# Optimization experiments

Hardware: AMD Instinct MI355X
Metric: run time of the kernel (lower is better)

Reference implementation:

```python
import jax, jax.numpy as jnp
import numpy as np

S, D = 8192, 2048      # sequence length, feature dim (input_size)
H, E, K, L = 64, 64, 2, 64  # gate hidden, expert count, top-k, expert layer_size
EPS = 1e-12            # torch F.normalize eps


def setup_inputs() -> dict:
    key = jax.random.key(0)
    ks = jax.random.split(key, 5)
    x = jax.random.normal(ks[0], (S, D), dtype=jnp.float32)
    # torch nn.Linear weights have shape [out_features, in_features]
    Wg_in = jax.random.normal(ks[1], (H, D), dtype=jnp.float32) * 0.02   # gate.input
    Wg_lin = jax.random.normal(ks[2], (E, H), dtype=jnp.float32) * 0.02  # gate.linear
    Wg_out = jax.random.normal(ks[3], (1, S), dtype=jnp.float32) * 0.02  # gate.output
    We = jax.random.normal(ks[4], (E, L, D), dtype=jnp.float32) * 0.02   # expert weight bank
    return {"x": x, "Wg_in": Wg_in, "Wg_lin": Wg_lin, "Wg_out": Wg_out, "We": We}


def reference(x, Wg_in, Wg_lin, Wg_out, We):
    # --- SparseGate (eval mode: dropout = identity) ---
    h = x @ Wg_in.T                         # [S, H]
    logits = h @ Wg_lin.T                   # [S, E]
    scores = (logits.T @ Wg_out.T)[:, 0]    # Linear(S,1) applied to [E,S] -> [E]
    topv, idx = jax.lax.top_k(scores, K)    # global top-k experts for whole input
    g = jax.nn.softmax(topv)                # softmax over the k selected logits

    # --- dispatch to k selected experts (FFNN: Linear -> normalize(-1) -> GELU) ---
    Wsel = We[idx]                          # [K, L, D]
    z = jnp.einsum('sd,kld->ksl', x, Wsel)  # [K, S, L]
    z = z / jnp.maximum(jnp.linalg.norm(z, axis=-1, keepdims=True), EPS)
    z = jax.nn.gelu(z, approximate=False)   # torch GELU default is exact erf

    # --- weighted combine: sum_k g_k * expert_k(x) ---
    return jnp.einsum('k,ksl->sl', g, z)    # [S, L]
```

## Files before the change

kernel.cpp:

```cpp
#include <hip/hip_runtime.h>
#include <hip/hip_bf16.h>
#include <math.h>

#define D_DIM 2048
#define L_DIM 64
#define E_NUM 64
#define H_DIM 64

typedef float f32x4_t __attribute__((ext_vector_type(4)));
typedef __bf16 bf16x8_t __attribute__((ext_vector_type(8)));

#define WS_UPART 0u
#define WS_U     (128u * 2048u * 4u)
#define WS_V     (WS_U + 2048u * 4u)
#define WS_META  (WS_V + 256u)
#define WS_WB    (WS_META + 64u)

__global__ void k_upart(const float* __restrict__ x, const float* __restrict__ wout,
                        float* __restrict__ upart) {
  const int d4 = (blockIdx.x * 256 + threadIdx.x) * 4;
  const int s0 = blockIdx.y * 64;
  const float* xp = x + (size_t)s0 * D_DIM + d4;
  float4 acc = make_float4(0.f, 0.f, 0.f, 0.f);
#pragma unroll 8
  for (int i = 0; i < 64; ++i) {
    const float w = wout[s0 + i];
    const float4 xv = *reinterpret_cast<const float4*>(xp + (size_t)i * D_DIM);
    acc.x += xv.x * w; acc.y += xv.y * w; acc.z += xv.z * w; acc.w += xv.w * w;
  }
  *reinterpret_cast<float4*>(upart + (size_t)blockIdx.y * D_DIM + d4) = acc;
}

__global__ void k_ufinish(const float* __restrict__ upart, float* __restrict__ u) {
  const int d = blockIdx.x * 256 + threadIdx.x;
  float s = 0.f;
#pragma unroll 8
  for (int c = 0; c < 128; ++c) s += upart[(size_t)c * D_DIM + d];
  u[d] = s;
}

__global__ void k_v(const float* __restrict__ wg_in, const float* __restrict__ u,
                    float* __restrict__ v) {
  const int h = blockIdx.x;
  const int t = threadIdx.x;
  const float4* wr = reinterpret_cast<const float4*>(wg_in + (size_t)h * D_DIM);
  const float4* ur = reinterpret_cast<const float4*>(u);
  float s = 0.f;
#pragma unroll
  for (int i = t; i < 512; i += 256) {
    const float4 a = wr[i];
    const float4 b = ur[i];
    s += a.x * b.x + a.y * b.y + a.z * b.z + a.w * b.w;
  }
  __shared__ float red[4];
#pragma unroll
  for (int off = 32; off; off >>= 1) s += __shfl_down(s, off, 64);
  if ((t & 63) == 0) red[t >> 6] = s;
  __syncthreads();
  if (t == 0) v[h] = red[0] + red[1] + red[2] + red[3];
}

__global__ void k_gate(const float* __restrict__ wg_lin, const float* __restrict__ v,
                       int* __restrict__ sel, float* __restrict__ g) {
  __shared__ float vv[H_DIM];
  __shared__ float sc[E_NUM];
  const int t = threadIdx.x;
  vv[t] = v[t];
  __syncthreads();
  float s = 0.f;
#pragma unroll 8
  for (int hh = 0; hh < H_DIM; ++hh) s += wg_lin[t * H_DIM + hh] * vv[hh];
  sc[t] = s;
  __syncthreads();
  if (t == 0) {
    int b1 = 0; float m1 = sc[0];
    for (int e = 1; e < E_NUM; ++e) { if (sc[e] > m1) { m1 = sc[e]; b1 = e; } }
    int b2 = -1; float m2 = -3.4e38f;
    for (int e = 0; e < E_NUM; ++e) {
      if (e != b1 && sc[e] > m2) { m2 = sc[e]; b2 = e; }
    }
    const float e2 = expf(m2 - m1);
    const float g0 = 1.0f / (1.0f + e2);
    sel[0] = b1; sel[1] = b2;
    g[0] = g0; g[1] = 1.0f - g0;
  }
}

__global__ void k_wb(const float* __restrict__ we, const int* __restrict__ sel,
                     __hip_bfloat16* __restrict__ wb) {
  const int n = blockIdx.x;
  const int e = sel[n >> 6];
  const int l = n & 63;
  const float* src = we + ((size_t)e * L_DIM + l) * D_DIM;
  const int t = threadIdx.x;
  const float4 a = reinterpret_cast<const float4*>(src)[2 * t];
  const float4 b = reinterpret_cast<const float4*>(src)[2 * t + 1];
  union { __hip_bfloat16 h[8]; uint4 u; } pk;
  pk.h[0] = __float2bfloat16(a.x); pk.h[1] = __float2bfloat16(a.y);
  pk.h[2] = __float2bfloat16(a.z); pk.h[3] = __float2bfloat16(a.w);
  pk.h[4] = __float2bfloat16(b.x); pk.h[5] = __float2bfloat16(b.y);
  pk.h[6] = __float2bfloat16(b.z); pk.h[7] = __float2bfloat16(b.w);
  reinterpret_cast<uint4*>(wb + (size_t)n * D_DIM)[t] = pk.u;
}

__device__ __forceinline__ void async_ld16(const void* gp, void* lp) {
  __builtin_amdgcn_global_load_lds(
      (const __attribute__((address_space(1))) unsigned int*)gp,
      (__attribute__((address_space(3))) unsigned int*)lp, 16, 0, 0);
}

__device__ __forceinline__ float gelu_f(float v) {
  return 0.5f * v * (1.0f + erff(v * 0.70710678118654752440f));
}

#define STG_BYTES 20992

__global__ __launch_bounds__(1024) void k_moe_gemm(
    const float* __restrict__ x, const __hip_bfloat16* __restrict__ wb,
    const float* __restrict__ gw, float* __restrict__ out) {
  __shared__ __align__(16) unsigned char lds[4 * STG_BYTES];

  const int tid = threadIdx.x;
  const int kg = tid >> 8;
  const int lt = tid & 255;
  const int wc = (tid >> 6) & 3;
  const int lane = tid & 63;
  const int m0 = blockIdx.x * 32;
  const float g0 = gw[0], g1 = gw[1];

  unsigned char* ldsA0 = lds + kg * STG_BYTES;
  unsigned char* ldsB0 = ldsA0 + 32 * 144;

  const int ar = lt >> 3, ac = lt & 7;
  const float* gA = x + (size_t)(m0 + ar) * D_DIM + kg * 512 + ac * 8;
  unsigned char* ldsAw = ldsA0 + ar * 144 + ac * 16;

  const int fr = lane & 15, fq = lane >> 4;

  f32x4_t acc00 = {0.f, 0.f, 0.f, 0.f};
  f32x4_t acc01 = acc00, acc10 = acc00, acc11 = acc00;

  for (int kk = 0; kk < 8; ++kk) {
    const int k0 = kg * 512 + kk * 64;
    if (kk) __syncthreads();
    const float4 a0 = *reinterpret_cast<const float4*>(gA + kk * 64);
    const float4 a1 = *reinterpret_cast<const float4*>(gA + kk * 64 + 4);
    union { __hip_bfloat16 h[8]; uint4 u; } pk;
    pk.h[0] = __float2bfloat16(a0.x); pk.h[1] = __float2bfloat16(a0.y);
    pk.h[2] = __float2bfloat16(a0.z); pk.h[3] = __float2bfloat16(a0.w);
    pk.h[4] = __float2bfloat16(a1.x); pk.h[5] = __float2bfloat16(a1.y);
    pk.h[6] = __float2bfloat16(a1.z); pk.h[7] = __float2bfloat16(a1.w);
    *reinterpret_cast<uint4*>(ldsAw) = pk.u;
#pragma unroll
    for (int i = 0; i < 4; ++i) {
      const int c = i * 256 + lt;
      const int r = c >> 3, p = c & 7;
      const int kc = p ^ (r & 7);
      async_ld16(wb + (size_t)r * D_DIM + k0 + kc * 8, ldsB0 + c * 16);
    }
    __syncthreads();
    union fragu { uint4 u; bf16x8_t v; };
    fragu af[2][2], bfr[2][2];
#pragma unroll
    for (int mt = 0; mt < 2; ++mt)
#pragma unroll
      for (int ks = 0; ks < 2; ++ks)
        af[mt][ks].u = *reinterpret_cast<const uint4*>(
            ldsA0 + (mt * 16 + fr) * 144 + ks * 64 + fq * 16);
#pragma unroll
    for (int nt = 0; nt < 2; ++nt)
#pragma unroll
      for (int ks = 0; ks < 2; ++ks) {
        const int r = wc * 32 + nt * 16 + fr;
        const int kq = ks * 4 + fq;
        bfr[nt][ks].u = *reinterpret_cast<const uint4*>(
            ldsB0 + r * 128 + ((kq ^ (r & 7)) * 16));
      }
    acc00 = __builtin_amdgcn_mfma_f32_16x16x32_bf16(af[0][0].v, bfr[0][0].v, acc00, 0, 0, 0);
    acc00 = __builtin_amdgcn_mfma_f32_16x16x32_bf16(af[0][1].v, bfr[0][1].v, acc00, 0, 0, 0);
    acc01 = __builtin_amdgcn_mfma_f32_16x16x32_bf16(af[0][0].v, bfr[1][0].v, acc01, 0, 0, 0);
    acc01 = __builtin_amdgcn_mfma_f32_16x16x32_bf16(af[0][1].v, bfr[1][1].v, acc01, 0, 0, 0);
    acc10 = __builtin_amdgcn_mfma_f32_16x16x32_bf16(af[1][0].v, bfr[0][0].v, acc10, 0, 0, 0);
    acc10 = __builtin_amdgcn_mfma_f32_16x16x32_bf16(af[1][1].v, bfr[0][1].v, acc10, 0, 0, 0);
    acc11 = __builtin_amdgcn_mfma_f32_16x16x32_bf16(af[1][0].v, bfr[1][0].v, acc11, 0, 0, 0);
    acc11 = __builtin_amdgcn_mfma_f32_16x16x32_bf16(af[1][1].v, bfr[1][1].v, acc11, 0, 0, 0);
  }
  __syncthreads();
  {
    float* z = reinterpret_cast<float*>(lds) + kg * (32 * 132);
    const int colbase = wc * 32 + fr;
#pragma unroll
    for (int reg = 0; reg < 4; ++reg) {
      const int r0 = fq * 4 + reg;
      z[r0 * 132 + colbase]             = acc00[reg];
      z[r0 * 132 + colbase + 16]        = acc01[reg];
      z[(16 + r0) * 132 + colbase]      = acc10[reg];
      z[(16 + r0) * 132 + colbase + 16] = acc11[reg];
    }
  }
  __syncthreads();
  {
    float* zb = reinterpret_cast<float*>(lds);
    const int r = tid >> 5;
    const int cb = (tid & 31) * 4;
    const int o = r * 132 + cb;
    f32x4_t s = *reinterpret_cast<f32x4_t*>(zb + o)
              + *reinterpret_cast<f32x4_t*>(zb + 1 * 4224 + o)
              + *reinterpret_cast<f32x4_t*>(zb + 2 * 4224 + o)
              + *reinterpret_cast<f32x4_t*>(zb + 3 * 4224 + o);
    *reinterpret_cast<f32x4_t*>(zb + o) = s;
  }
  __syncthreads();
  float* z = reinterpret_cast<float*>(lds);
  float* ps = reinterpret_cast<float*>(lds + 4 * 16896);
  if (tid < 256) {
    const int r = tid >> 3, seg = tid & 7;
    float s = 0.f;
#pragma unroll
    for (int i2 = 0; i2 < 16; ++i2) {
      const float t2 = z[r * 132 + seg * 16 + i2];
      s += t2 * t2;
    }
    ps[r * 8 + seg] = s;
  }
  __syncthreads();
  if (tid < 256) {
    const int r = tid >> 3, j = tid & 7;
    const float s0 = ps[r * 8 + 0] + ps[r * 8 + 1] + ps[r * 8 + 2] + ps[r * 8 + 3];
    const float s1 = ps[r * 8 + 4] + ps[r * 8 + 5] + ps[r * 8 + 6] + ps[r * 8 + 7];
    const float i0 = 1.0f / fmaxf(sqrtf(s0), 1e-12f);
    const float i1 = 1.0f / fmaxf(sqrtf(s1), 1e-12f);
    float o[8];
#pragma unroll
    for (int i2 = 0; i2 < 8; ++i2) {
      const int c = j * 8 + i2;
      const float za = z[r * 132 + c] * i0;
      const float zb = z[r * 132 + 64 + c] * i1;
      o[i2] = g0 * gelu_f(za) + g1 * gelu_f(zb);
    }
    float4* op = reinterpret_cast<float4*>(out + (size_t)(m0 + r) * 64 + j * 8);
    op[0] = make_float4(o[0], o[1], o[2], o[3]);
    op[1] = make_float4(o[4], o[5], o[6], o[7]);
  }
}

extern "C" void kernel_launch(void* const* d_in, const int* in_sizes, int n_in,
                              void* d_out, int out_size, void* d_ws, size_t ws_size,
                              hipStream_t stream) {
  (void)in_sizes; (void)n_in; (void)out_size; (void)ws_size;
  const float* x      = (const float*)d_in[0];
  const float* wg_in  = (const float*)d_in[1];
  const float* wg_lin = (const float*)d_in[2];
  const float* wg_out = (const float*)d_in[3];
  const float* we     = (const float*)d_in[4];
  float* out = (float*)d_out;
  char* ws = (char*)d_ws;

  float* upart = (float*)(ws + WS_UPART);
  float* u     = (float*)(ws + WS_U);
  float* v     = (float*)(ws + WS_V);
  int*   sel   = (int*)(ws + WS_META);
  float* g     = (float*)(ws + WS_META + 8);
  __hip_bfloat16* wb = (__hip_bfloat16*)(ws + WS_WB);

  k_upart  <<<dim3(2, 128), 256, 0, stream>>>(x, wg_out, upart);
  k_ufinish<<<8, 256, 0, stream>>>(upart, u);
  k_v      <<<64, 256, 0, stream>>>(wg_in, u, v);
  k_gate   <<<1, 64, 0, stream>>>(wg_lin, v, sel, g);
  k_wb     <<<128, 256, 0, stream>>>(we, sel, wb);
  k_moe_gemm<<<256, 1024, 0, stream>>>(x, wb, g, out);
}
```

Before: 159.3 us.

## Precompute bf16 copy of x in reduction pass and feed it to expert GEMM

```diff
diff --git a/kernel.cpp b/kernel.cpp
--- a/kernel.cpp
+++ b/kernel.cpp
@@ -8,6 +8,7 @@
 #define H_DIM 64
 
 typedef float f32x4_t __attribute__((ext_vector_type(4)));
+typedef unsigned int u32x4_t __attribute__((ext_vector_type(4)));
 typedef __bf16 bf16x8_t __attribute__((ext_vector_type(8)));
 
 #define WS_UPART 0u
@@ -15,18 +16,24 @@
 #define WS_V     (WS_U + 2048u * 4u)
 #define WS_META  (WS_V + 256u)
 #define WS_WB    (WS_META + 64u)
+#define WS_XB    (WS_WB + 128u * 2048u * 2u)
 
 __global__ void k_upart(const float* __restrict__ x, const float* __restrict__ wout,
-                        float* __restrict__ upart) {
+                        float* __restrict__ upart, __hip_bfloat16* __restrict__ xb) {
   const int d4 = (blockIdx.x * 256 + threadIdx.x) * 4;
   const int s0 = blockIdx.y * 64;
   const float* xp = x + (size_t)s0 * D_DIM + d4;
   float4 acc = make_float4(0.f, 0.f, 0.f, 0.f);
-#pragma unroll 8
+#pragma unroll 4
   for (int i = 0; i < 64; ++i) {
     const float w = wout[s0 + i];
-    const float4 xv = *reinterpret_cast<const float4*>(xp + (size_t)i * D_DIM);
-    acc.x += xv.x * w; acc.y += xv.y * w; acc.z += xv.z * w; acc.w += xv.w * w;
+    const f32x4_t xv = __builtin_nontemporal_load(
+        reinterpret_cast<const f32x4_t*>(xp + (size_t)i * D_DIM));
+    acc.x += xv[0] * w; acc.y += xv[1] * w; acc.z += xv[2] * w; acc.w += xv[3] * w;
+    union { __hip_bfloat16 h[4]; uint2 u; } pk;
+    pk.h[0] = __float2bfloat16(xv[0]); pk.h[1] = __float2bfloat16(xv[1]);
+    pk.h[2] = __float2bfloat16(xv[2]); pk.h[3] = __float2bfloat16(xv[3]);
+    *reinterpret_cast<uint2*>(xb + (size_t)(s0 + i) * D_DIM + d4) = pk.u;
   }
   *reinterpret_cast<float4*>(upart + (size_t)blockIdx.y * D_DIM + d4) = acc;
 }
@@ -113,10 +120,10 @@
   return 0.5f * v * (1.0f + erff(v * 0.70710678118654752440f));
 }
 
-#define STG_BYTES 20992
+#define STG_BYTES 20480
 
 __global__ __launch_bounds__(1024) void k_moe_gemm(
-    const float* __restrict__ x, const __hip_bfloat16* __restrict__ wb,
+    const __hip_bfloat16* __restrict__ xb, const __hip_bfloat16* __restrict__ wb,
     const float* __restrict__ gw, float* __restrict__ out) {
   __shared__ __align__(16) unsigned char lds[4 * STG_BYTES];
 
@@ -129,11 +136,12 @@
   const float g0 = gw[0], g1 = gw[1];
 
   unsigned char* ldsA0 = lds + kg * STG_BYTES;
-  unsigned char* ldsB0 = ldsA0 + 32 * 144;
-
-  const int ar = lt >> 3, ac = lt & 7;
-  const float* gA = x + (size_t)(m0 + ar) * D_DIM + kg * 512 + ac * 8;
-  unsigned char* ldsAw = ldsA0 + ar * 144 + ac * 16;
+  unsigned char* ldsB0 = ldsA0 + 32 * 128;
+
+  const int sar = lt >> 3, sap = lt & 7;
+  const int sakc = sap ^ (sar & 7);
+  const __hip_bfloat16* gA = xb + (size_t)(m0 + sar) * D_DIM + kg * 512 + sakc * 8;
+  unsigned char* ldsAw = ldsA0 + lt * 16;
 
   const int fr = lane & 15, fq = lane >> 4;
 
@@ -143,14 +151,8 @@
   for (int kk = 0; kk < 8; ++kk) {
     const int k0 = kg * 512 + kk * 64;
     if (kk) __syncthreads();
-    const float4 a0 = *reinterpret_cast<const float4*>(gA + kk * 64);
-    const float4 a1 = *reinterpret_cast<const float4*>(gA + kk * 64 + 4);
-    union { __hip_bfloat16 h[8]; uint4 u; } pk;
-    pk.h[0] = __float2bfloat16(a0.x); pk.h[1] = __float2bfloat16(a0.y);
-    pk.h[2] = __float2bfloat16(a0.z); pk.h[3] = __float2bfloat16(a0.w);
-    pk.h[4] = __float2bfloat16(a1.x); pk.h[5] = __float2bfloat16(a1.y);
-    pk.h[6] = __float2bfloat16(a1.z); pk.h[7] = __float2bfloat16(a1.w);
-    *reinterpret_cast<uint4*>(ldsAw) = pk.u;
+    const u32x4_t av = __builtin_nontemporal_load(
+        reinterpret_cast<const u32x4_t*>(gA + kk * 64));
 #pragma unroll
     for (int i = 0; i < 4; ++i) {
       const int c = i * 256 + lt;
@@ -158,15 +160,19 @@
       const int kc = p ^ (r & 7);
       async_ld16(wb + (size_t)r * D_DIM + k0 + kc * 8, ldsB0 + c * 16);
     }
+    *reinterpret_cast<u32x4_t*>(ldsAw) = av;
     __syncthreads();
     union fragu { uint4 u; bf16x8_t v; };
     fragu af[2][2], bfr[2][2];
 #pragma unroll
     for (int mt = 0; mt < 2; ++mt)
 #pragma unroll
-      for (int ks = 0; ks < 2; ++ks)
+      for (int ks = 0; ks < 2; ++ks) {
+        const int ar2 = mt * 16 + fr;
+        const int kq = ks * 4 + fq;
         af[mt][ks].u = *reinterpret_cast<const uint4*>(
-            ldsA0 + (mt * 16 + fr) * 144 + ks * 64 + fq * 16);
+            ldsA0 + ar2 * 128 + ((kq ^ (ar2 & 7)) * 16));
+      }
 #pragma unroll
     for (int nt = 0; nt < 2; ++nt)
 #pragma unroll
@@ -235,8 +241,8 @@
     for (int i2 = 0; i2 < 8; ++i2) {
       const int c = j * 8 + i2;
       const float za = z[r * 132 + c] * i0;
-      const float zb = z[r * 132 + 64 + c] * i1;
-      o[i2] = g0 * gelu_f(za) + g1 * gelu_f(zb);
+      const float zb2 = z[r * 132 + 64 + c] * i1;
+      o[i2] = g0 * gelu_f(za) + g1 * gelu_f(zb2);
     }
     float4* op = reinterpret_cast<float4*>(out + (size_t)(m0 + r) * 64 + j * 8);
     op[0] = make_float4(o[0], o[1], o[2], o[3]);
@@ -262,11 +268,12 @@
   int*   sel   = (int*)(ws + WS_META);
   float* g     = (float*)(ws + WS_META + 8);
   __hip_bfloat16* wb = (__hip_bfloat16*)(ws + WS_WB);
-
-  k_upart  <<<dim3(2, 128), 256, 0, stream>>>(x, wg_out, upart);
+  __hip_bfloat16* xb = (__hip_bfloat16*)(ws + WS_XB);
+
+  k_upart  <<<dim3(2, 128), 256, 0, stream>>>(x, wg_out, upart, xb);
   k_ufinish<<<8, 256, 0, stream>>>(upart, u);
   k_v      <<<64, 256, 0, stream>>>(wg_in, u, v);
   k_gate   <<<1, 64, 0, stream>>>(wg_lin, v, sel, g);
   k_wb     <<<128, 256, 0, stream>>>(we, sel, wb);
-  k_moe_gemm<<<256, 1024, 0, stream>>>(x, wb, g, out);
-}
+  k_moe_gemm<<<256, 1024, 0, stream>>>(xb, wb, g, out);
+}
```

Result: slower. 169.1 us (+6.2%).
